# Kernel optimization log

Measured on AMD Instinct MI355X. Metric: run time of the kernel, lower is better.

## Reference

```python
import jax, jax.numpy as jnp
import numpy as np

K1, K2 = 0.01, 0.03
DATA_RANGE = 1.0
EPS = 1e-6


def setup_inputs() -> dict:
    key = jax.random.key(0)
    k1, k2, k3 = jax.random.split(key, 3)
    B, C, H, W = 4, 3, 256, 176
    S, M = 5, 18
    X = jax.random.normal(k1, (B, C, H, W), dtype=jnp.float32)
    Y = jax.random.normal(k2, (B, C, H, W), dtype=jnp.float32)
    bp_mask = jax.random.uniform(k3, (B, S, M, H, W), dtype=jnp.float32)
    return {"X": X, "Y": Y, "bp_mask": bp_mask}


def reference(X, Y, bp_mask):
    # Rescale from [-1, 1] to [0, 1]
    X = (X + 1.0) / 2.0
    Y = (Y + 1.0) / 2.0
    C1 = (K1 * DATA_RANGE) ** 2
    C2 = (K2 * DATA_RANGE) ** 2

    # Normalized mask weights: [B, S, M, H, W]
    msum = bp_mask.sum(axis=(-2, -1), keepdims=True)
    w = bp_mask / (msum + EPS)

    # Masked first / second moments -> [B, S, M, C], no repeated 6D tensors
    mu1 = jnp.einsum('bchw,bsmhw->bsmc', X, w)
    mu2 = jnp.einsum('bchw,bsmhw->bsmc', Y, w)
    mu11 = jnp.einsum('bchw,bsmhw->bsmc', X * X, w)
    mu22 = jnp.einsum('bchw,bsmhw->bsmc', Y * Y, w)
    mu12 = jnp.einsum('bchw,bsmhw->bsmc', X * Y, w)

    mu1_sq = mu1 * mu1
    mu2_sq = mu2 * mu2
    mu1_mu2 = mu1 * mu2
    sigma1_sq = mu11 - mu1_sq
    sigma2_sq = mu22 - mu2_sq
    sigma12 = mu12 - mu1_mu2

    cs = (2.0 * sigma12 + C2) / (sigma1_sq + sigma2_sq + C2)
    ssim = (2.0 * mu1_mu2 + C1) / (mu1_sq + mu2_sq + C1) * cs
    # nonnegative_ssim=True
    ssim = jax.nn.relu(ssim)
    cs = jax.nn.relu(cs)

    # Mean over merged (M, C) axis -> [B, S]
    cs_batch = cs.mean(axis=(2, 3))
    ssim_batch = ssim.mean(axis=(2, 3))

    msssim = jnp.prod(cs_batch[:, :-1], axis=1) * ssim_batch[:, -1]
    return msssim.mean()
```

## Files before the change

### kernel.cpp

```cpp
#include <hip/hip_runtime.h>

#define B_  4
#define C_  3
#define S_  5
#define M_  18
#define HW4 11264
#define SPLIT 11
#define TPB 256
#define CHUNK4 (HW4/SPLIT)
#define ITERS (CHUNK4/TPB)
#define NPLANE (B_*S_*M_)

__global__ __launch_bounds__(TPB) void moments_kernel(
    const float4* __restrict__ X, const float4* __restrict__ Y,
    const float4* __restrict__ Mk, float* __restrict__ part) {
  int bid   = blockIdx.x;
  int plane = bid / SPLIT;
  int chunk = bid - plane * SPLIT;
  int b     = plane / (S_ * M_);

  const float4* mp = Mk + (size_t)plane * HW4;
  const float4* xp = X  + (size_t)b * (C_ * HW4);
  const float4* yp = Y  + (size_t)b * (C_ * HW4);

  int base = chunk * CHUNK4 + (int)threadIdx.x;

  float v[16];
#pragma unroll
  for (int j = 0; j < 16; ++j) v[j] = 0.f;

#pragma unroll
  for (int it = 0; it < ITERS; ++it) {
    int i = base + it * TPB;
    float4 w = mp[i];
    float4 xv[C_], yv[C_];
#pragma unroll
    for (int c = 0; c < C_; ++c) { xv[c] = xp[c * HW4 + i]; yv[c] = yp[c * HW4 + i]; }

    float w4[4]     = { w.x, w.y, w.z, w.w };
    float x4[C_][4] = { {xv[0].x, xv[0].y, xv[0].z, xv[0].w},
                        {xv[1].x, xv[1].y, xv[1].z, xv[1].w},
                        {xv[2].x, xv[2].y, xv[2].z, xv[2].w} };
    float y4[C_][4] = { {yv[0].x, yv[0].y, yv[0].z, yv[0].w},
                        {yv[1].x, yv[1].y, yv[1].z, yv[1].w},
                        {yv[2].x, yv[2].y, yv[2].z, yv[2].w} };
#pragma unroll
    for (int k = 0; k < 4; ++k) {
      float wk = w4[k];
      v[0] += wk;
#pragma unroll
      for (int c = 0; c < C_; ++c) {
        float xs = fmaf(x4[c][k], 0.5f, 0.5f);
        float ys = fmaf(y4[c][k], 0.5f, 0.5f);
        float wx = wk * xs, wy = wk * ys;
        v[1 + c*5 + 0] = fmaf(wk, xs, v[1 + c*5 + 0]);
        v[1 + c*5 + 1] = fmaf(wk, ys, v[1 + c*5 + 1]);
        v[1 + c*5 + 2] = fmaf(wx, xs, v[1 + c*5 + 2]);
        v[1 + c*5 + 3] = fmaf(wy, ys, v[1 + c*5 + 3]);
        v[1 + c*5 + 4] = fmaf(wx, ys, v[1 + c*5 + 4]);
      }
    }
  }

#pragma unroll
  for (int off = 32; off > 0; off >>= 1) {
#pragma unroll
    for (int j = 0; j < 16; ++j) v[j] += __shfl_xor(v[j], off);
  }

  __shared__ float red[TPB/64][16];
  int lane = threadIdx.x & 63;
  int wv   = threadIdx.x >> 6;
  if (lane == 0) {
#pragma unroll
    for (int j = 0; j < 16; ++j) red[wv][j] = v[j];
  }
  __syncthreads();
  if (threadIdx.x < 16) {
    float s = (red[0][threadIdx.x] + red[1][threadIdx.x]) +
              (red[2][threadIdx.x] + red[3][threadIdx.x]);
    part[(size_t)bid * 16 + threadIdx.x] = s;
  }
}

__global__ __launch_bounds__(384) void finalize_kernel(
    const float* __restrict__ part, float* __restrict__ out) {
  __shared__ float csS[NPLANE], ssS[NPLANE];
  __shared__ double csb[B_*S_], ssb[B_*S_];
  int t = threadIdx.x;

  if (t < NPLANE) {
    double s[16];
#pragma unroll
    for (int j = 0; j < 16; ++j) s[j] = 0.0;
    for (int ch = 0; ch < SPLIT; ++ch) {
      const float* p = part + (size_t)(t * SPLIT + ch) * 16;
#pragma unroll
      for (int j = 0; j < 16; ++j) s[j] += (double)p[j];
    }
    const double C1d = 1e-4, C2d = 9e-4;
    double inv = 1.0 / (s[0] + 1e-6);
    double csAcc = 0.0, ssAcc = 0.0;
#pragma unroll
    for (int c = 0; c < C_; ++c) {
      double mu1  = s[1 + c*5 + 0] * inv;
      double mu2  = s[1 + c*5 + 1] * inv;
      double mu11 = s[1 + c*5 + 2] * inv;
      double mu22 = s[1 + c*5 + 3] * inv;
      double mu12 = s[1 + c*5 + 4] * inv;
      double m1s = mu1*mu1, m2s = mu2*mu2, m12 = mu1*mu2;
      double sig1  = mu11 - m1s;
      double sig2  = mu22 - m2s;
      double sig12 = mu12 - m12;
      double cs   = (2.0*sig12 + C2d) / (sig1 + sig2 + C2d);
      double ssim = (2.0*m12 + C1d) / (m1s + m2s + C1d) * cs;
      if (cs   < 0.0) cs   = 0.0;
      if (ssim < 0.0) ssim = 0.0;
      csAcc += cs; ssAcc += ssim;
    }
    csS[t] = (float)csAcc;
    ssS[t] = (float)ssAcc;
  }
  __syncthreads();

  if (t < B_*S_) {
    double cb = 0.0, sb = 0.0;
    for (int m = 0; m < M_; ++m) { cb += (double)csS[t*M_ + m]; sb += (double)ssS[t*M_ + m]; }
    csb[t] = cb / (double)(M_*C_);
    ssb[t] = sb / (double)(M_*C_);
  }
  __syncthreads();

  if (t == 0) {
    double acc = 0.0;
    for (int b = 0; b < B_; ++b) {
      double p = ssb[b*S_ + (S_-1)];
      for (int s = 0; s < S_-1; ++s) p *= csb[b*S_ + s];
      acc += p;
    }
    out[0] = (float)(acc / (double)B_);
  }
}

extern "C" void kernel_launch(void* const* d_in, const int* in_sizes, int n_in,
                              void* d_out, int out_size, void* d_ws, size_t ws_size,
                              hipStream_t stream) {
  (void)in_sizes; (void)n_in; (void)out_size; (void)ws_size;
  const float4* X  = (const float4*)d_in[0];
  const float4* Y  = (const float4*)d_in[1];
  const float4* Mk = (const float4*)d_in[2];
  float* part = (float*)d_ws;
  float* out  = (float*)d_out;

  hipLaunchKernelGGL(moments_kernel, dim3(NPLANE*SPLIT), dim3(TPB), 0, stream,
                     X, Y, Mk, part);
  hipLaunchKernelGGL(finalize_kernel, dim3(1), dim3(384), 0, stream, part, out);
}
```

Measured before the change: 119.7 us.

## Share X/Y tiles across six mask planes via double-buffered LDS

Each block now handles six mask planes of the same batch at once, one wave per plane. The six waves cooperatively load and rescale the six X/Y channel chunks into a double-buffered shared tile. This cuts redundant global reads of X and Y, which were previously refetched for every mask plane. In exchange it adds a block-wide barrier on every iteration, doubles the chunk split, and changes the block ordering so blocks are grouped by chunk, which may help L2 reuse.

```diff
diff --git a/kernel.cpp b/kernel.cpp
--- a/kernel.cpp
+++ b/kernel.cpp
@@ -5,53 +5,80 @@
 #define S_  5
 #define M_  18
 #define HW4 11264
-#define SPLIT 11
-#define TPB 256
+#define G_  6
+#define NGI (S_*M_/G_)
+#define SPLIT 22
 #define CHUNK4 (HW4/SPLIT)
-#define ITERS (CHUNK4/TPB)
+#define ITERS (CHUNK4/64)
+#define TPB (G_*64)
 #define NPLANE (B_*S_*M_)
+#define NBLK (B_*NGI*SPLIT)
 
 __global__ __launch_bounds__(TPB) void moments_kernel(
     const float4* __restrict__ X, const float4* __restrict__ Y,
     const float4* __restrict__ Mk, float* __restrict__ part) {
+  __shared__ float4 tile[2][6][64];
+
   int bid   = blockIdx.x;
-  int plane = bid / SPLIT;
-  int chunk = bid - plane * SPLIT;
-  int b     = plane / (S_ * M_);
+  int chunk = bid / (B_ * NGI);
+  int r     = bid - chunk * (B_ * NGI);
+  int b     = r & 3;
+  int gi    = r >> 2;
+  int s     = gi / 3;
+  int mg    = gi - s * 3;
+  int wv    = threadIdx.x >> 6;
+  int lane  = threadIdx.x & 63;
+  int plane = (b * S_ + s) * M_ + mg * G_ + wv;
 
   const float4* mp = Mk + (size_t)plane * HW4;
-  const float4* xp = X  + (size_t)b * (C_ * HW4);
-  const float4* yp = Y  + (size_t)b * (C_ * HW4);
-
-  int base = chunk * CHUNK4 + (int)threadIdx.x;
+  const float4* sp = (wv < 3) ? (X + (size_t)b * (C_ * HW4) + (size_t)wv * HW4)
+                              : (Y + (size_t)b * (C_ * HW4) + (size_t)(wv - 3) * HW4);
+  int base = chunk * CHUNK4;
 
   float v[16];
 #pragma unroll
   for (int j = 0; j < 16; ++j) v[j] = 0.f;
 
+  {
+    float4 sv = sp[base + lane];
+    sv.x = fmaf(sv.x, 0.5f, 0.5f); sv.y = fmaf(sv.y, 0.5f, 0.5f);
+    sv.z = fmaf(sv.z, 0.5f, 0.5f); sv.w = fmaf(sv.w, 0.5f, 0.5f);
+    tile[0][wv][lane] = sv;
+  }
+
 #pragma unroll
   for (int it = 0; it < ITERS; ++it) {
-    int i = base + it * TPB;
+    int buf = it & 1;
+    int i   = base + it * 64 + lane;
     float4 w = mp[i];
-    float4 xv[C_], yv[C_];
+
+    __syncthreads();
+
+    if (it + 1 < ITERS) {
+      float4 sv = sp[i + 64];
+      sv.x = fmaf(sv.x, 0.5f, 0.5f); sv.y = fmaf(sv.y, 0.5f, 0.5f);
+      sv.z = fmaf(sv.z, 0.5f, 0.5f); sv.w = fmaf(sv.w, 0.5f, 0.5f);
+      tile[buf ^ 1][wv][lane] = sv;
+    }
+
+    float4 xs4[C_], ys4[C_];
 #pragma unroll
-    for (int c = 0; c < C_; ++c) { xv[c] = xp[c * HW4 + i]; yv[c] = yp[c * HW4 + i]; }
+    for (int c = 0; c < C_; ++c) { xs4[c] = tile[buf][c][lane]; ys4[c] = tile[buf][3 + c][lane]; }
 
     float w4[4]     = { w.x, w.y, w.z, w.w };
-    float x4[C_][4] = { {xv[0].x, xv[0].y, xv[0].z, xv[0].w},
-                        {xv[1].x, xv[1].y, xv[1].z, xv[1].w},
-                        {xv[2].x, xv[2].y, xv[2].z, xv[2].w} };
-    float y4[C_][4] = { {yv[0].x, yv[0].y, yv[0].z, yv[0].w},
-                        {yv[1].x, yv[1].y, yv[1].z, yv[1].w},
-                        {yv[2].x, yv[2].y, yv[2].z, yv[2].w} };
+    float xsv[C_][4] = { {xs4[0].x, xs4[0].y, xs4[0].z, xs4[0].w},
+                         {xs4[1].x, xs4[1].y, xs4[1].z, xs4[1].w},
+                         {xs4[2].x, xs4[2].y, xs4[2].z, xs4[2].w} };
+    float ysv[C_][4] = { {ys4[0].x, ys4[0].y, ys4[0].z, ys4[0].w},
+                         {ys4[1].x, ys4[1].y, ys4[1].z, ys4[1].w},
+                         {ys4[2].x, ys4[2].y, ys4[2].z, ys4[2].w} };
 #pragma unroll
     for (int k = 0; k < 4; ++k) {
       float wk = w4[k];
       v[0] += wk;
 #pragma unroll
       for (int c = 0; c < C_; ++c) {
-        float xs = fmaf(x4[c][k], 0.5f, 0.5f);
-        float ys = fmaf(y4[c][k], 0.5f, 0.5f);
+        float xs = xsv[c][k], ys = ysv[c][k];
         float wx = wk * xs, wy = wk * ys;
         v[1 + c*5 + 0] = fmaf(wk, xs, v[1 + c*5 + 0]);
         v[1 + c*5 + 1] = fmaf(wk, ys, v[1 + c*5 + 1]);
@@ -68,18 +95,12 @@
     for (int j = 0; j < 16; ++j) v[j] += __shfl_xor(v[j], off);
   }
 
-  __shared__ float red[TPB/64][16];
-  int lane = threadIdx.x & 63;
-  int wv   = threadIdx.x >> 6;
   if (lane == 0) {
-#pragma unroll
-    for (int j = 0; j < 16; ++j) red[wv][j] = v[j];
-  }
-  __syncthreads();
-  if (threadIdx.x < 16) {
-    float s = (red[0][threadIdx.x] + red[1][threadIdx.x]) +
-              (red[2][threadIdx.x] + red[3][threadIdx.x]);
-    part[(size_t)bid * 16 + threadIdx.x] = s;
+    float4* dst = (float4*)(part + (size_t)(plane * SPLIT + chunk) * 16);
+    dst[0] = make_float4(v[0],  v[1],  v[2],  v[3]);
+    dst[1] = make_float4(v[4],  v[5],  v[6],  v[7]);
+    dst[2] = make_float4(v[8],  v[9],  v[10], v[11]);
+    dst[3] = make_float4(v[12], v[13], v[14], v[15]);
   }
 }
 
@@ -94,9 +115,12 @@
 #pragma unroll
     for (int j = 0; j < 16; ++j) s[j] = 0.0;
     for (int ch = 0; ch < SPLIT; ++ch) {
-      const float* p = part + (size_t)(t * SPLIT + ch) * 16;
-#pragma unroll
-      for (int j = 0; j < 16; ++j) s[j] += (double)p[j];
+      const float4* p = (const float4*)(part + (size_t)(t * SPLIT + ch) * 16);
+      float4 q0 = p[0], q1 = p[1], q2 = p[2], q3 = p[3];
+      s[0]+=q0.x;  s[1]+=q0.y;  s[2]+=q0.z;  s[3]+=q0.w;
+      s[4]+=q1.x;  s[5]+=q1.y;  s[6]+=q1.z;  s[7]+=q1.w;
+      s[8]+=q2.x;  s[9]+=q2.y;  s[10]+=q2.z; s[11]+=q2.w;
+      s[12]+=q3.x; s[13]+=q3.y; s[14]+=q3.z; s[15]+=q3.w;
     }
     const double C1d = 1e-4, C2d = 9e-4;
     double inv = 1.0 / (s[0] + 1e-6);
@@ -152,7 +176,7 @@
   float* part = (float*)d_ws;
   float* out  = (float*)d_out;
 
-  hipLaunchKernelGGL(moments_kernel, dim3(NPLANE*SPLIT), dim3(TPB), 0, stream,
+  hipLaunchKernelGGL(moments_kernel, dim3(NBLK), dim3(TPB), 0, stream,
                      X, Y, Mk, part);
   hipLaunchKernelGGL(finalize_kernel, dim3(1), dim3(384), 0, stream, part, out);
 }
```

Measured after the change: 131.5 us. 9.8% more time.
